# Kernel tuning notes

Hardware: AMD Instinct MI355X
Metric: run time of the kernel (lower is better)

The kernel has to match this reference:

```python
import jax, jax.numpy as jnp
import numpy as np

VOCAB = 1_000_000
D = 128
N = 16384
NSAMP = 8192
TEMP = 0.05
L2_NORM = True


def _l2n(x):
    return x / (jnp.linalg.norm(x, axis=-1, keepdims=True) + 1e-12)


def setup_inputs() -> dict:
    key = jax.random.key(0)
    k1, k2, k3, k4, k5 = jax.random.split(key, 5)
    inputs = jax.random.normal(k1, (N, D), dtype=jnp.float32)
    target_ids = jax.random.randint(k2, (N, 1), 0, VOCAB, dtype=jnp.int64) if jax.config.jax_enable_x64 else jax.random.randint(k2, (N, 1), 0, VOCAB, dtype=jnp.int32)
    neg_ids = jax.random.randint(k3, (NSAMP,), 0, VOCAB, dtype=jnp.int32)
    weights = jax.random.uniform(k4, (N,), dtype=jnp.float32)
    projection = jax.random.normal(k5, (VOCAB, D), dtype=jnp.float32) * 0.02
    return {"inputs": inputs, "target_ids": target_ids, "neg_ids": neg_ids,
            "weights": weights, "projection": projection}


def reference(inputs, target_ids, neg_ids, weights, projection):
    # mask = (target_ids != -100).sum(-1).bool(); instead of dynamic boolean
    # indexing, fold the mask into the per-example weights (same weighted mean).
    valid = ((target_ids != -100).sum(axis=-1) > 0).astype(inputs.dtype)  # [N]
    tgt = jnp.clip(target_ids[:, 0], 0, VOCAB - 1)  # safe gather for masked rows

    pos_emb = projection[tgt]       # [N, D] gather
    neg_emb = projection[neg_ids]   # [S, D] gather

    x = inputs
    if L2_NORM:
        x = _l2n(x)
        pos_emb = _l2n(pos_emb)
        neg_emb = _l2n(neg_emb)

    pos_logit = jnp.einsum('nd,nd->n', x, pos_emb) / TEMP          # [N]
    neg_logits = jnp.einsum('nd,sd->ns', x, neg_emb) / TEMP        # [N, S]

    logits = jnp.concatenate([pos_logit[:, None], neg_logits], axis=-1)  # [N, 1+S]
    logZ = jax.scipy.special.logsumexp(logits, axis=-1)            # [N]
    ce = logZ - pos_logit                                          # -log p(pos)

    w = weights * valid
    loss = jnp.sum(ce * w) / jnp.maximum(jnp.sum(w), 1e-12)
    return loss
```

## Files before the change

kernel.cpp:

```cpp
#include <hip/hip_runtime.h>
#include <hip/hip_bf16.h>
#include <stdint.h>
#include <math.h>

#define VOCAB 1000000
#define D 128
#define NROWS 16384
#define NSAMP 8192
#define SSPLIT 16
#define K1F 28.853900817779268f
#define LOG2EF 1.4426950408889634f

#define XF_OFF 0u
#define EF_OFF 2097152u
#define PL_OFF 3145728u
#define SCX_OFF 3211264u
#define PS_OFF 3276800u
#define FP_OFF 4325376u
#define CNT_OFF 4326400u

typedef __attribute__((ext_vector_type(4))) int i32x4;
typedef __attribute__((ext_vector_type(16))) int i32x16;

#if __has_builtin(__builtin_amdgcn_exp2f)
#define EXP2(x) __builtin_amdgcn_exp2f(x)
#else
#define EXP2(x) exp2f(x)
#endif

__device__ __forceinline__ void gl_lds16(const void* g, void* l) {
  __builtin_amdgcn_global_load_lds(
      (const __attribute__((address_space(1))) unsigned int*)g,
      (__attribute__((address_space(3))) unsigned int*)l, 16, 0, 0);
}

__device__ __forceinline__ float wave_sum(float v) {
#pragma unroll
  for (int o = 1; o < 64; o <<= 1) v += __shfl_xor(v, o);
  return v;
}

__device__ __forceinline__ void store_frag_i8(char* __restrict__ base, int row,
                                              int lane, int bx, int by) {
  const int d = lane * 2;
  const int kk = d >> 5, sub = (d & 31) >> 4, j = d & 15;
  const int tile = row >> 5, lt = (sub << 5) | (row & 31);
  char* dst = base + (((size_t)(tile * 4 + kk) * 64 + lt) * 16 + j);
  dst[0] = (char)bx;
  dst[1] = (char)by;
}

__global__ __launch_bounds__(256) void prep_kernel(
    const float* __restrict__ x, const int* __restrict__ tgt,
    const int* __restrict__ nid, const float* __restrict__ proj,
    char* __restrict__ xf, char* __restrict__ ef,
    float* __restrict__ pl, float* __restrict__ scx,
    unsigned int* __restrict__ cnt) {
  if (blockIdx.x == 0 && threadIdx.x == 0) *cnt = 0u;
  const int wave = threadIdx.x >> 6, lane = threadIdx.x & 63;
  if (blockIdx.x < 1024) {
    const int n0 = blockIdx.x * 16 + wave * 4;
    int tg[4];
    float2 xr[4], pr[4];
#pragma unroll
    for (int i = 0; i < 4; ++i) {
      const int t = tgt[n0 + i];
      tg[i] = t < 0 ? 0 : (t > VOCAB - 1 ? VOCAB - 1 : t);
      xr[i] = *reinterpret_cast<const float2*>(x + (size_t)(n0 + i) * D + lane * 2);
    }
#pragma unroll
    for (int i = 0; i < 4; ++i)
      pr[i] = *reinterpret_cast<const float2*>(proj + (size_t)tg[i] * D + lane * 2);
#pragma unroll
    for (int i = 0; i < 4; ++i) {
      float sx = xr[i].x * xr[i].x + xr[i].y * xr[i].y;
      float sp = pr[i].x * pr[i].x + pr[i].y * pr[i].y;
      float dt = xr[i].x * pr[i].x + xr[i].y * pr[i].y;
      float mx = fmaxf(fabsf(xr[i].x), fabsf(xr[i].y));
#pragma unroll
      for (int o = 1; o < 64; o <<= 1) {
        sx += __shfl_xor(sx, o);
        sp += __shfl_xor(sp, o);
        dt += __shfl_xor(dt, o);
        mx = fmaxf(mx, __shfl_xor(mx, o));
      }
      const float norm = sqrtf(sx) + 1e-12f;
      if (lane == 0) {
        pl[n0 + i] = dt / (norm * (sqrtf(sp) + 1e-12f)) * 20.0f;
        scx[n0 + i] = K1F * (mx + 1e-20f) / (16129.0f * norm);
      }
      const float qs = 127.0f / (mx + 1e-20f);
      store_frag_i8(xf, n0 + i, lane, (int)rintf(xr[i].x * qs),
                    (int)rintf(xr[i].y * qs));
    }
  } else {
    const int s0 = (blockIdx.x - 1024) * 16 + wave * 4;
    float2 er[4];
#pragma unroll
    for (int i = 0; i < 4; ++i) {
      const int id = nid[s0 + i];
      er[i] = *reinterpret_cast<const float2*>(proj + (size_t)id * D + lane * 2);
    }
#pragma unroll
    for (int i = 0; i < 4; ++i) {
      const float qs =
          127.0f / (sqrtf(wave_sum(er[i].x * er[i].x + er[i].y * er[i].y)) + 1e-12f);
      store_frag_i8(ef, s0 + i, lane, (int)rintf(er[i].x * qs),
                    (int)rintf(er[i].y * qs));
    }
  }
}

__global__ __launch_bounds__(256, 4) void flash_kernel(
    const char* __restrict__ xf, const char* __restrict__ ef,
    const float* __restrict__ scx, float* __restrict__ psum) {
  __shared__ __align__(16) char lds[2][8192];
  const int tid = threadIdx.x, wave = tid >> 6, lane = tid & 63;
  const int nb = blockIdx.x & 63, ss = blockIdx.x >> 6;
  const int nbase = nb * 256 + wave * 64;

  i32x4 bq[2][4];
#pragma unroll
  for (int nf = 0; nf < 2; ++nf) {
    const char* p = xf + ((size_t)(nb * 8 + wave * 2 + nf) * 4096) + lane * 16;
#pragma unroll
    for (int kk = 0; kk < 4; ++kk)
      bq[nf][kk] = *reinterpret_cast<const i32x4*>(p + kk * 1024);
  }
  const float scx0 = scx[nbase + (lane & 31)];
  const float scx1 = scx[nbase + 32 + (lane & 31)];

  const char* esrc = ef + (size_t)ss * 65536;
  float acc0 = 0.f, acc1 = 0.f;

  {
    const char* g = esrc + tid * 16;
    char* l = &lds[0][0] + tid * 16;
    gl_lds16(g, l);
    gl_lds16(g + 4096, l + 4096);
  }
  __syncthreads();

  for (int st = 0; st < 8; ++st) {
    if (st < 7) {
      const char* g = esrc + (size_t)(st + 1) * 8192 + tid * 16;
      char* l = &lds[(st + 1) & 1][0] + tid * 16;
      gl_lds16(g, l);
      gl_lds16(g + 4096, l + 4096);
    }
    const char* cb = &lds[st & 1][0];
#pragma unroll
    for (int tt = 0; tt < 2; ++tt) {
      i32x16 c0, c1;
#pragma unroll
      for (int r = 0; r < 16; ++r) { c0[r] = 0; c1[r] = 0; }
      const char* ab = cb + tt * 4096 + lane * 16;
#pragma unroll
      for (int kk = 0; kk < 4; ++kk) {
        i32x4 a = *reinterpret_cast<const i32x4*>(ab + kk * 1024);
        c0 = __builtin_amdgcn_mfma_i32_32x32x32_i8(a, bq[0][kk], c0, 0, 0, 0);
        c1 = __builtin_amdgcn_mfma_i32_32x32x32_i8(a, bq[1][kk], c1, 0, 0, 0);
      }
      float e0[16], e1[16];
#pragma unroll
      for (int r = 0; r < 16; ++r) {
        e0[r] = EXP2((float)c0[r] * scx0);
        e1[r] = EXP2((float)c1[r] * scx1);
      }
#pragma unroll
      for (int s2 = 8; s2; s2 >>= 1)
#pragma unroll
        for (int r = 0; r < s2; ++r) { e0[r] += e0[r + s2]; e1[r] += e1[r + s2]; }
      acc0 += e0[0];
      acc1 += e1[0];
    }
    __syncthreads();
  }

  acc0 += __shfl_xor(acc0, 32);
  acc1 += __shfl_xor(acc1, 32);
  if (lane < 32) {
    psum[(size_t)ss * NROWS + nbase + lane] = acc0;
    psum[(size_t)ss * NROWS + nbase + 32 + lane] = acc1;
  }
}

__global__ __launch_bounds__(256) void finish_kernel(
    const float* __restrict__ psum, const float* __restrict__ pl,
    const int* __restrict__ tgt, const float* __restrict__ wts,
    float* __restrict__ fin, unsigned int* __restrict__ cnt,
    float* __restrict__ out) {
  const int n = blockIdx.x * 256 + threadIdx.x;
  float tot = 0.f;
#pragma unroll
  for (int s = 0; s < SSPLIT; ++s) tot += psum[(size_t)s * NROWS + n];
  const float p = pl[n];
  tot += EXP2(p * LOG2EF);
  const float ce = logf(tot) - p;
  const float w = wts[n] * (tgt[n] != -100 ? 1.f : 0.f);
  float a = wave_sum(ce * w);
  float b = wave_sum(w);
  __shared__ float sa[4], sb[4];
  __shared__ int last;
  const int wave = threadIdx.x >> 6, lane = threadIdx.x & 63;
  if (lane == 0) { sa[wave] = a; sb[wave] = b; }
  __syncthreads();
  if (threadIdx.x == 0) {
    __hip_atomic_store(&fin[blockIdx.x * 2], sa[0] + sa[1] + sa[2] + sa[3],
                       __ATOMIC_RELAXED, __HIP_MEMORY_SCOPE_AGENT);
    __hip_atomic_store(&fin[blockIdx.x * 2 + 1], sb[0] + sb[1] + sb[2] + sb[3],
                       __ATOMIC_RELAXED, __HIP_MEMORY_SCOPE_AGENT);
    const unsigned int old = __hip_atomic_fetch_add(cnt, 1u, __ATOMIC_ACQ_REL,
                                                    __HIP_MEMORY_SCOPE_AGENT);
    last = (old == 63u);
  }
  __syncthreads();
  if (last && threadIdx.x < 64) {
    const float A = wave_sum(__hip_atomic_load(&fin[threadIdx.x * 2],
                                               __ATOMIC_RELAXED,
                                               __HIP_MEMORY_SCOPE_AGENT));
    const float B = wave_sum(__hip_atomic_load(&fin[threadIdx.x * 2 + 1],
                                               __ATOMIC_RELAXED,
                                               __HIP_MEMORY_SCOPE_AGENT));
    if (threadIdx.x == 0) out[0] = A / fmaxf(B, 1e-12f);
  }
}

extern "C" void kernel_launch(void* const* d_in, const int* in_sizes, int n_in,
                              void* d_out, int out_size, void* d_ws, size_t ws_size,
                              hipStream_t stream) {
  const float* x    = (const float*)d_in[0];
  const int*   tgt  = (const int*)d_in[1];
  const int*   nid  = (const int*)d_in[2];
  const float* wts  = (const float*)d_in[3];
  const float* proj = (const float*)d_in[4];
  float* out = (float*)d_out;
  char* ws = (char*)d_ws;
  char* xf = ws + XF_OFF;
  char* ef = ws + EF_OFF;
  float* pl   = (float*)(ws + PL_OFF);
  float* scx  = (float*)(ws + SCX_OFF);
  float* psum = (float*)(ws + PS_OFF);
  float* fin  = (float*)(ws + FP_OFF);
  unsigned int* cnt = (unsigned int*)(ws + CNT_OFF);

  hipLaunchKernelGGL(prep_kernel, dim3(1024 + 512), dim3(256), 0, stream,
                     x, tgt, nid, proj, xf, ef, pl, scx, cnt);
  hipLaunchKernelGGL(flash_kernel, dim3(64 * SSPLIT), dim3(256), 0, stream,
                     xf, ef, scx, psum);
  hipLaunchKernelGGL(finish_kernel, dim3(NROWS / 256), dim3(256), 0, stream,
                     psum, pl, tgt, wts, fin, cnt, out);
}
```

Before: 42.12 us.

## Fuse finish reduction into flash kernel via last-block atomic counters

Removes the separate finish kernel launch. Each flash block publishes its partial sums with atomic stores and bumps a per-row-block counter. The last of the 16 split blocks for a row block computes the cross-entropy terms, and a second counter picks the final block to write the loss. This saves one kernel launch and its dependency gap, at the cost of extra atomics and a serialized tail in the last blocks. The prep kernel now zeroes 1025 counter words, padded to avoid false sharing.

Result: slower. 55.88 us (+32.7%).

```diff
diff --git a/kernel.cpp b/kernel.cpp
--- a/kernel.cpp
+++ b/kernel.cpp
@@ -17,7 +17,8 @@
 #define SCX_OFF 3211264u
 #define PS_OFF 3276800u
 #define FP_OFF 4325376u
-#define CNT_OFF 4326400u
+#define PC_OFF 4326400u
+#define CNT2_OFF 4330496u
 
 typedef __attribute__((ext_vector_type(4))) int i32x4;
 typedef __attribute__((ext_vector_type(16))) int i32x16;
@@ -55,8 +56,10 @@
     const int* __restrict__ nid, const float* __restrict__ proj,
     char* __restrict__ xf, char* __restrict__ ef,
     float* __restrict__ pl, float* __restrict__ scx,
-    unsigned int* __restrict__ cnt) {
-  if (blockIdx.x == 0 && threadIdx.x == 0) *cnt = 0u;
+    unsigned int* __restrict__ zero_base) {
+  if (blockIdx.x == 0) {
+    for (int i = threadIdx.x; i < 1025; i += 256) zero_base[i] = 0u;
+  }
   const int wave = threadIdx.x >> 6, lane = threadIdx.x & 63;
   if (blockIdx.x < 1024) {
     const int n0 = blockIdx.x * 16 + wave * 4;
@@ -113,7 +116,11 @@
 
 __global__ __launch_bounds__(256, 4) void flash_kernel(
     const char* __restrict__ xf, const char* __restrict__ ef,
-    const float* __restrict__ scx, float* __restrict__ psum) {
+    const float* __restrict__ scx, const float* __restrict__ pl,
+    const int* __restrict__ tgt, const float* __restrict__ wts,
+    float* __restrict__ psum, float* __restrict__ fin,
+    unsigned int* __restrict__ percnt, unsigned int* __restrict__ cnt2,
+    float* __restrict__ out) {
   __shared__ __align__(16) char lds[2][8192];
   const int tid = threadIdx.x, wave = tid >> 6, lane = tid & 63;
   const int nb = blockIdx.x & 63, ss = blockIdx.x >> 6;
@@ -180,20 +187,28 @@
   acc0 += __shfl_xor(acc0, 32);
   acc1 += __shfl_xor(acc1, 32);
   if (lane < 32) {
-    psum[(size_t)ss * NROWS + nbase + lane] = acc0;
-    psum[(size_t)ss * NROWS + nbase + 32 + lane] = acc1;
-  }
-}
-
-__global__ __launch_bounds__(256) void finish_kernel(
-    const float* __restrict__ psum, const float* __restrict__ pl,
-    const int* __restrict__ tgt, const float* __restrict__ wts,
-    float* __restrict__ fin, unsigned int* __restrict__ cnt,
-    float* __restrict__ out) {
-  const int n = blockIdx.x * 256 + threadIdx.x;
+    __hip_atomic_store(&psum[(size_t)ss * NROWS + nbase + lane], acc0,
+                       __ATOMIC_RELAXED, __HIP_MEMORY_SCOPE_AGENT);
+    __hip_atomic_store(&psum[(size_t)ss * NROWS + nbase + 32 + lane], acc1,
+                       __ATOMIC_RELAXED, __HIP_MEMORY_SCOPE_AGENT);
+  }
+  __syncthreads();
+
+  __shared__ int ilast;
+  if (tid == 0) {
+    const unsigned int old = __hip_atomic_fetch_add(
+        &percnt[nb * 16], 1u, __ATOMIC_ACQ_REL, __HIP_MEMORY_SCOPE_AGENT);
+    ilast = (old == SSPLIT - 1);
+  }
+  __syncthreads();
+  if (!ilast) return;
+
+  const int n = nb * 256 + tid;
   float tot = 0.f;
 #pragma unroll
-  for (int s = 0; s < SSPLIT; ++s) tot += psum[(size_t)s * NROWS + n];
+  for (int s = 0; s < SSPLIT; ++s)
+    tot += __hip_atomic_load(&psum[(size_t)s * NROWS + n], __ATOMIC_RELAXED,
+                             __HIP_MEMORY_SCOPE_AGENT);
   const float p = pl[n];
   tot += EXP2(p * LOG2EF);
   const float ce = logf(tot) - p;
@@ -201,28 +216,29 @@
   float a = wave_sum(ce * w);
   float b = wave_sum(w);
   __shared__ float sa[4], sb[4];
-  __shared__ int last;
-  const int wave = threadIdx.x >> 6, lane = threadIdx.x & 63;
+  __shared__ int last2;
   if (lane == 0) { sa[wave] = a; sb[wave] = b; }
   __syncthreads();
-  if (threadIdx.x == 0) {
-    __hip_atomic_store(&fin[blockIdx.x * 2], sa[0] + sa[1] + sa[2] + sa[3],
-                       __ATOMIC_RELAXED, __HIP_MEMORY_SCOPE_AGENT);
-    __hip_atomic_store(&fin[blockIdx.x * 2 + 1], sb[0] + sb[1] + sb[2] + sb[3],
-                       __ATOMIC_RELAXED, __HIP_MEMORY_SCOPE_AGENT);
-    const unsigned int old = __hip_atomic_fetch_add(cnt, 1u, __ATOMIC_ACQ_REL,
-                                                    __HIP_MEMORY_SCOPE_AGENT);
-    last = (old == 63u);
-  }
-  __syncthreads();
-  if (last && threadIdx.x < 64) {
-    const float A = wave_sum(__hip_atomic_load(&fin[threadIdx.x * 2],
+  if (tid == 0) {
+    __hip_atomic_store(&fin[nb * 2], sa[0] + sa[1] + sa[2] + sa[3],
+                       __ATOMIC_RELAXED, __HIP_MEMORY_SCOPE_AGENT);
+    __hip_atomic_store(&fin[nb * 2 + 1], sb[0] + sb[1] + sb[2] + sb[3],
+                       __ATOMIC_RELAXED, __HIP_MEMORY_SCOPE_AGENT);
+  }
+  __syncthreads();
+  if (tid == 0) {
+    const unsigned int o2 = __hip_atomic_fetch_add(cnt2, 1u, __ATOMIC_ACQ_REL,
+                                                   __HIP_MEMORY_SCOPE_AGENT);
+    last2 = (o2 == 63u);
+  }
+  __syncthreads();
+  if (last2 && tid < 64) {
+    const float A = wave_sum(__hip_atomic_load(&fin[tid * 2], __ATOMIC_RELAXED,
+                                               __HIP_MEMORY_SCOPE_AGENT));
+    const float B = wave_sum(__hip_atomic_load(&fin[tid * 2 + 1],
                                                __ATOMIC_RELAXED,
                                                __HIP_MEMORY_SCOPE_AGENT));
-    const float B = wave_sum(__hip_atomic_load(&fin[threadIdx.x * 2 + 1],
-                                               __ATOMIC_RELAXED,
-                                               __HIP_MEMORY_SCOPE_AGENT));
-    if (threadIdx.x == 0) out[0] = A / fmaxf(B, 1e-12f);
+    if (tid == 0) out[0] = A / fmaxf(B, 1e-12f);
   }
 }
 
@@ -242,12 +258,11 @@
   float* scx  = (float*)(ws + SCX_OFF);
   float* psum = (float*)(ws + PS_OFF);
   float* fin  = (float*)(ws + FP_OFF);
-  unsigned int* cnt = (unsigned int*)(ws + CNT_OFF);
+  unsigned int* percnt = (unsigned int*)(ws + PC_OFF);
+  unsigned int* cnt2   = (unsigned int*)(ws + CNT2_OFF);
 
   hipLaunchKernelGGL(prep_kernel, dim3(1024 + 512), dim3(256), 0, stream,
-                     x, tgt, nid, proj, xf, ef, pl, scx, cnt);
+                     x, tgt, nid, proj, xf, ef, pl, scx, percnt);
   hipLaunchKernelGGL(flash_kernel, dim3(64 * SSPLIT), dim3(256), 0, stream,
-                     xf, ef, scx, psum);
-  hipLaunchKernelGGL(finish_kernel, dim3(NROWS / 256), dim3(256), 0, stream,
-                     psum, pl, tgt, wts, fin, cnt, out);
-}
+                     xf, ef, scx, pl, tgt, wts, psum, fin, percnt, cnt2, out);
+}
```

## Load negative-embedding fragments directly from global memory instead of LDS staging

Applied to the files above, without the earlier changes.

The flash kernel no longer stages the int8 negative-embedding tiles through double-buffered shared memory with async global-to-LDS copies and block barriers. Each wave now reads its MFMA A fragments straight from global memory (relying on L2/L1 caching, since all four waves read the same tile), and the loop is flattened to 16 tiles. This removes the __syncthreads and LDS traffic but gives up explicit prefetch overlap and shared reuse, so it depends on cache hits and on the compiler hiding load latency.

Result: slower. 43.97 us (+4.4%).

```diff
diff --git a/kernel.cpp b/kernel.cpp
--- a/kernel.cpp
+++ b/kernel.cpp
@@ -27,12 +27,6 @@
 #else
 #define EXP2(x) exp2f(x)
 #endif
-
-__device__ __forceinline__ void gl_lds16(const void* g, void* l) {
-  __builtin_amdgcn_global_load_lds(
-      (const __attribute__((address_space(1))) unsigned int*)g,
-      (__attribute__((address_space(3))) unsigned int*)l, 16, 0, 0);
-}
 
 __device__ __forceinline__ float wave_sum(float v) {
 #pragma unroll
@@ -114,7 +108,6 @@
 __global__ __launch_bounds__(256, 4) void flash_kernel(
     const char* __restrict__ xf, const char* __restrict__ ef,
     const float* __restrict__ scx, float* __restrict__ psum) {
-  __shared__ __align__(16) char lds[2][8192];
   const int tid = threadIdx.x, wave = tid >> 6, lane = tid & 63;
   const int nb = blockIdx.x & 63, ss = blockIdx.x >> 6;
   const int nbase = nb * 256 + wave * 64;
@@ -130,51 +123,38 @@
   const float scx0 = scx[nbase + (lane & 31)];
   const float scx1 = scx[nbase + 32 + (lane & 31)];
 
-  const char* esrc = ef + (size_t)ss * 65536;
+  const char* esrc = ef + (size_t)ss * 65536 + lane * 16;
   float acc0 = 0.f, acc1 = 0.f;
 
-  {
-    const char* g = esrc + tid * 16;
-    char* l = &lds[0][0] + tid * 16;
-    gl_lds16(g, l);
-    gl_lds16(g + 4096, l + 4096);
-  }
-  __syncthreads();
-
-  for (int st = 0; st < 8; ++st) {
-    if (st < 7) {
-      const char* g = esrc + (size_t)(st + 1) * 8192 + tid * 16;
-      char* l = &lds[(st + 1) & 1][0] + tid * 16;
-      gl_lds16(g, l);
-      gl_lds16(g + 4096, l + 4096);
-    }
-    const char* cb = &lds[st & 1][0];
-#pragma unroll
-    for (int tt = 0; tt < 2; ++tt) {
-      i32x16 c0, c1;
-#pragma unroll
-      for (int r = 0; r < 16; ++r) { c0[r] = 0; c1[r] = 0; }
-      const char* ab = cb + tt * 4096 + lane * 16;
-#pragma unroll
-      for (int kk = 0; kk < 4; ++kk) {
-        i32x4 a = *reinterpret_cast<const i32x4*>(ab + kk * 1024);
-        c0 = __builtin_amdgcn_mfma_i32_32x32x32_i8(a, bq[0][kk], c0, 0, 0, 0);
-        c1 = __builtin_amdgcn_mfma_i32_32x32x32_i8(a, bq[1][kk], c1, 0, 0, 0);
-      }
-      float e0[16], e1[16];
-#pragma unroll
-      for (int r = 0; r < 16; ++r) {
-        e0[r] = EXP2((float)c0[r] * scx0);
-        e1[r] = EXP2((float)c1[r] * scx1);
-      }
-#pragma unroll
-      for (int s2 = 8; s2; s2 >>= 1)
-#pragma unroll
-        for (int r = 0; r < s2; ++r) { e0[r] += e0[r + s2]; e1[r] += e1[r + s2]; }
-      acc0 += e0[0];
-      acc1 += e1[0];
-    }
-    __syncthreads();
+  for (int t = 0; t < 16; ++t) {
+    const char* ab = esrc + (size_t)t * 4096;
+    const i32x4 a0 = *reinterpret_cast<const i32x4*>(ab);
+    const i32x4 a1 = *reinterpret_cast<const i32x4*>(ab + 1024);
+    const i32x4 a2 = *reinterpret_cast<const i32x4*>(ab + 2048);
+    const i32x4 a3 = *reinterpret_cast<const i32x4*>(ab + 3072);
+    i32x16 c0, c1;
+#pragma unroll
+    for (int r = 0; r < 16; ++r) { c0[r] = 0; c1[r] = 0; }
+    c0 = __builtin_amdgcn_mfma_i32_32x32x32_i8(a0, bq[0][0], c0, 0, 0, 0);
+    c1 = __builtin_amdgcn_mfma_i32_32x32x32_i8(a0, bq[1][0], c1, 0, 0, 0);
+    c0 = __builtin_amdgcn_mfma_i32_32x32x32_i8(a1, bq[0][1], c0, 0, 0, 0);
+    c1 = __builtin_amdgcn_mfma_i32_32x32x32_i8(a1, bq[1][1], c1, 0, 0, 0);
+    c0 = __builtin_amdgcn_mfma_i32_32x32x32_i8(a2, bq[0][2], c0, 0, 0, 0);
+    c1 = __builtin_amdgcn_mfma_i32_32x32x32_i8(a2, bq[1][2], c1, 0, 0, 0);
+    c0 = __builtin_amdgcn_mfma_i32_32x32x32_i8(a3, bq[0][3], c0, 0, 0, 0);
+    c1 = __builtin_amdgcn_mfma_i32_32x32x32_i8(a3, bq[1][3], c1, 0, 0, 0);
+    float e0[16], e1[16];
+#pragma unroll
+    for (int r = 0; r < 16; ++r) {
+      e0[r] = EXP2((float)c0[r] * scx0);
+      e1[r] = EXP2((float)c1[r] * scx1);
+    }
+#pragma unroll
+    for (int s2 = 8; s2; s2 >>= 1)
+#pragma unroll
+      for (int r = 0; r < s2; ++r) { e0[r] += e0[r + s2]; e1[r] += e1[r + s2]; }
+    acc0 += e0[0];
+    acc1 += e1[0];
   }
 
   acc0 += __shfl_xor(acc0, 32);
```
